# Kernel optimization log

Hardware: AMD Instinct MI355X
Metric: run time of the kernel (lower is better)

Reference implementation:

```python
import jax, jax.numpy as jnp
import numpy as np
from jax import lax

EPS = 1e-10

def _ln(x, g, b):
    m = x.mean(-1, keepdims=True)
    v = x.var(-1, keepdims=True)
    return (x - m) / jnp.sqrt(v + 1e-5) * g + b

def _gather(t, idx):
    # t: (B, HW, c), idx: (B, HW, d) -> (B, HW, d, c); out[n,i,k,:] = t[n, idx[n,i,k], :]
    return jax.vmap(lambda tn, In: tn[In])(t, idx)

def setup_inputs() -> dict:
    key = jax.random.key(0)
    ks = jax.random.split(key, 20)
    b, v, c, d, h, w, hid, ksz = 2, 2, 128, 64, 64, 64, 256, 5
    hw = h * w
    Bf = b * v  # v_1 == 1 target view per reference view
    std = 0.02
    return {
        'features_mv': jax.random.normal(ks[0], (b, v, c, h, w), jnp.float32),
        'warp_indices': jax.random.randint(ks[1], (Bf, hw, d), 0, hw, jnp.int32),
        'depth_prob': jax.random.uniform(ks[2], (Bf, hw, d), jnp.float32),
        'ln1_g': jnp.ones((c,), jnp.float32), 'ln1_b': jnp.zeros((c,), jnp.float32),
        'wq': jax.random.normal(ks[3], (c, c), jnp.float32) * std, 'bq': jnp.zeros((c,), jnp.float32),
        'wk': jax.random.normal(ks[4], (c, c), jnp.float32) * std, 'bk': jnp.zeros((c,), jnp.float32),
        'wv': jax.random.normal(ks[5], (c, c), jnp.float32) * std, 'bv': jnp.zeros((c,), jnp.float32),
        'k_pe': jax.random.normal(ks[6], (1, 1, d), jnp.float32) * std,
        'v_pe': jax.random.normal(ks[7], (1, 1, d), jnp.float32) * std,
        'rpe': jax.random.normal(ks[8], (1, 1, d), jnp.float32) * std,
        'proj_w': jax.random.normal(ks[9], (c, c), jnp.float32) * std, 'proj_b': jnp.zeros((c,), jnp.float32),
        'ln2_g': jnp.ones((c,), jnp.float32), 'ln2_b': jnp.zeros((c,), jnp.float32),
        'fc1_w': jax.random.normal(ks[10], (c, hid), jnp.float32) * std, 'fc1_b': jnp.zeros((hid,), jnp.float32),
        'dw_w': jax.random.normal(ks[11], (hid, 1, ksz, ksz), jnp.float32) * std, 'dw_b': jnp.zeros((hid,), jnp.float32),
        'fc2_w': jax.random.normal(ks[12], (hid, c), jnp.float32) * std, 'fc2_b': jnp.zeros((c,), jnp.float32),
    }

def reference(features_mv, warp_indices, depth_prob, ln1_g, ln1_b, wq, bq, wk, bk, wv, bv,
              k_pe, v_pe, rpe, proj_w, proj_b, ln2_g, ln2_b, fc1_w, fc1_b, dw_w, dw_b, fc2_w, fc2_b):
    b, v, c, h, w = features_mv.shape
    hw = h * w
    hid = fc1_w.shape[1]
    scale = c ** (-0.5)  # num_heads = 1 -> head_dim = dim

    # (b v) (h w) c
    x = features_mv.reshape(b * v, c, hw).transpose(0, 2, 1)
    shortcut = x
    xn = _ln(x, ln1_g, ln1_b)
    q = xn @ wq + bq
    k = xn @ wk + bk
    vv = xn @ wv + bv

    # nn pairing: v=2, v_1=1 -> each reference view attends the other view
    Q = (q.reshape(b, v, hw, c) * scale).reshape(b * v, hw, c)
    K = k.reshape(b, v, hw, c)[:, ::-1].reshape(b * v, hw, c)
    V = vv.reshape(b, v, hw, c)[:, ::-1].reshape(b * v, hw, c)

    # SMM_QmK: cost[n,i,k] = sum_c Q[n,i,c] * K[n, idx[n,i,k], c]
    Kg = _gather(K, warp_indices)                       # (B, hw, d, c)
    cost = jnp.einsum('bic,bikc->bik', Q, Kg)
    Q_pe = Q.sum(-1, keepdims=True)                     # (B, hw, 1)
    cost = cost + Q_pe * k_pe + rpe                     # broadcast (1,1,d)

    # (Sim_UNet similarity refinement omitted: UNetModel source unavailable; identity here)
    attn = jax.nn.softmax(cost, axis=-1)
    attn = attn * depth_prob
    attn = (attn + EPS) / (attn.sum(-1, keepdims=True) + EPS)

    # SMM_AmV: out[n,i,c] = sum_k attn[n,i,k] * V[n, idx[n,i,k], c]
    Vg = _gather(V, warp_indices)                       # (B, hw, d, c)
    out = jnp.einsum('bik,bikc->bic', attn, Vg)
    out = out + (attn * v_pe).sum(-1, keepdims=True)

    # projection + residual (v_1 == 1 so B == b*v)
    x = shortcut + (out @ proj_w + proj_b)

    # ConvFFN residual branch
    xn2 = _ln(x, ln2_g, ln2_b)
    y = jax.nn.gelu(xn2 @ fc1_w + fc1_b, approximate=False)
    yi = y.transpose(0, 2, 1).reshape(b * v, hid, h, w)
    yc = lax.conv_general_dilated(yi, dw_w, (1, 1), 'SAME', feature_group_count=hid,
                                  dimension_numbers=('NCHW', 'OIHW', 'NCHW'))
    yc = jax.nn.gelu(yc + dw_b[None, :, None, None], approximate=False)
    y = y + yc.reshape(b * v, hid, hw).transpose(0, 2, 1)
    y = y @ fc2_w + fc2_b
    return x + y
```

## Files before the change

### kernel.cpp

```cpp
#include <hip/hip_runtime.h>
#include <math.h>

#define TOK   16384
#define HW    4096
#define C     128
#define D     64
#define HID   256

constexpr float LN_EPS = 1e-5f;
constexpr float EPS_R  = 1e-10f;
constexpr float QSCALE = 0.08838834764831845f;

typedef __attribute__((ext_vector_type(8))) short  bf16x8;
typedef __attribute__((ext_vector_type(4))) float  f32x4;
#define MFMA16(a, b, c) __builtin_amdgcn_mfma_f32_16x16x32_bf16((a), (b), (c), 0, 0, 0)

__device__ __forceinline__ float bflo(unsigned u) { return __uint_as_float(u << 16); }
__device__ __forceinline__ float bfhi(unsigned u) { return __uint_as_float(u & 0xffff0000u); }
__device__ __forceinline__ float bfu(unsigned short u) { return __uint_as_float((unsigned)u << 16); }
__device__ __forceinline__ unsigned short f2bf(float f) {
  unsigned u = __float_as_uint(f);
  unsigned r = (u + 0x7fffu + ((u >> 16) & 1u)) >> 16;
  return (unsigned short)r;
}
__device__ __forceinline__ float gelu_exact(float x) {
  return 0.5f * x * (1.0f + erff(x * 0.7071067811865476f));
}

__global__ __launch_bounds__(256) void k_prep(const float* __restrict__ wq,
    const float* __restrict__ wk, const float* __restrict__ wv,
    const float* __restrict__ pw, const float* __restrict__ f1w,
    const float* __restrict__ f2w, unsigned short* __restrict__ wt) {
  int id = blockIdx.x * 256 + threadIdx.x;
  if (id < 16384) {
    int n = id >> 7, k = id & 127;
    wt[id] = f2bf(wq[k * 128 + n]);
  } else if (id < 32768) {
    int e = id - 16384; int n = e >> 7, k = e & 127;
    wt[id] = f2bf(wk[k * 128 + n]);
  } else if (id < 49152) {
    int e = id - 32768; int n = e >> 7, k = e & 127;
    wt[id] = f2bf(wv[k * 128 + n]);
  } else if (id < 65536) {
    int e = id - 49152; int n = e >> 7, k = e & 127;
    wt[id] = f2bf(pw[k * 128 + n]);
  } else if (id < 98304) {
    int e = id - 65536; int n = e >> 7, k = e & 127;
    wt[id] = f2bf(f1w[k * 256 + n]);
  } else if (id < 131072) {
    int e = id - 98304; int n = e >> 8, k = e & 255;
    wt[id] = f2bf(f2w[k * 128 + n]);
  }
}

__global__ __launch_bounds__(256) void k_ln1(const float* __restrict__ feat,
    const float* __restrict__ g, const float* __restrict__ b,
    unsigned short* __restrict__ xnb, float* __restrict__ xtm) {
  __shared__ float tile[64][C + 1];
  int t0 = blockIdx.x * 64;
  int n = t0 / HW, i0 = t0 % HW;
  int tid = threadIdx.x;
  const float* fb = feat + (size_t)n * C * HW;
  for (int e = tid; e < 64 * C; e += 256) {
    int ch = e >> 6, ii = e & 63;
    tile[ii][ch] = fb[(size_t)ch * HW + i0 + ii];
  }
  __syncthreads();
  int wave = tid >> 6, lane = tid & 63;
  for (int tkn = wave; tkn < 64; tkn += 4) {
    float a0 = tile[tkn][lane];
    float a1 = tile[tkn][lane + 64];
    float s = a0 + a1;
    for (int off = 32; off; off >>= 1) s += __shfl_xor(s, off, 64);
    float mean = s * (1.0f / 128.0f);
    float d0 = a0 - mean, d1 = a1 - mean;
    float v = d0 * d0 + d1 * d1;
    for (int off = 32; off; off >>= 1) v += __shfl_xor(v, off, 64);
    float rstd = rsqrtf(v * (1.0f / 128.0f) + LN_EPS);
    size_t ro = (size_t)(t0 + tkn) * C;
    xnb[ro + lane]      = f2bf(d0 * rstd * g[lane] + b[lane]);
    xnb[ro + lane + 64] = f2bf(d1 * rstd * g[lane + 64] + b[lane + 64]);
    xtm[ro + lane]      = a0;
    xtm[ro + lane + 64] = a1;
  }
}

__global__ __launch_bounds__(256) void k_qkv(const unsigned short* __restrict__ xnb,
    const unsigned short* __restrict__ wt,
    const float* __restrict__ bq, const float* __restrict__ bk,
    const float* __restrict__ bv, float* __restrict__ q,
    unsigned short* __restrict__ ksw, unsigned short* __restrict__ vsw) {
  int w = threadIdx.x >> 6, lane = threadIdx.x & 63;
  int q4 = lane >> 4, m = lane & 15;
  int t0 = blockIdx.x * 64 + w * 16;
  int wsel = blockIdx.y;
  const unsigned short* Wt = wt + wsel * 16384;
  const unsigned short* ap = xnb + (size_t)(t0 + m) * C + q4 * 8;
  bf16x8 a[4];
  #pragma unroll
  for (int ks = 0; ks < 4; ks++) a[ks] = *(const bf16x8*)(ap + ks * 32);
  f32x4 acc[8];
  #pragma unroll
  for (int nt = 0; nt < 8; nt++) acc[nt] = (f32x4){0.f, 0.f, 0.f, 0.f};
  #pragma unroll
  for (int nt = 0; nt < 8; nt++) {
    const unsigned short* bp = Wt + (size_t)(nt * 16 + m) * C + q4 * 8;
    #pragma unroll
    for (int ks = 0; ks < 4; ks++) {
      bf16x8 bfrag = *(const bf16x8*)(bp + ks * 32);
      acc[nt] = MFMA16(a[ks], bfrag, acc[nt]);
    }
  }
  if (wsel == 0) {
    #pragma unroll
    for (int nt = 0; nt < 8; nt++) {
      int col = nt * 16 + m;
      float bb = bq[col];
      #pragma unroll
      for (int reg = 0; reg < 4; reg++) {
        int row = t0 + q4 * 4 + reg;
        q[(size_t)row * C + col] = (acc[nt][reg] + bb) * QSCALE;
      }
    }
  } else {
    const float* B = (wsel == 1) ? bk : bv;
    unsigned short* O = (wsel == 1) ? ksw : vsw;
    int n = t0 >> 12, i0 = t0 & 4095;
    int tsw = ((n ^ 1) << 12) + i0;
    #pragma unroll
    for (int nt = 0; nt < 8; nt++) {
      int col = nt * 16 + m;
      float bb = B[col];
      #pragma unroll
      for (int reg = 0; reg < 4; reg++) {
        int row = tsw + q4 * 4 + reg;
        O[(size_t)row * C + col] = f2bf(acc[nt][reg] + bb);
      }
    }
  }
}

__global__ __launch_bounds__(256) void k_attn(const float* __restrict__ q,
    const unsigned short* __restrict__ ksw, const unsigned short* __restrict__ vsw,
    const int* __restrict__ widx, const float* __restrict__ dprob,
    const float* __restrict__ kpe, const float* __restrict__ vpe,
    const float* __restrict__ rpe, unsigned short* __restrict__ aoutb) {
  int lane = threadIdx.x & 63;
  int wave = threadIdx.x >> 6;
  int token = blockIdx.x * 4 + wave;
  int n = token >> 12;
  const unsigned short* Kb = ksw + (size_t)n * HW * C;
  const unsigned short* Vb = vsw + (size_t)n * HW * C;
  int g = lane >> 3, s = lane & 7;
  float qreg[16];
  const float* qp = q + (size_t)token * C + s * 16;
  #pragma unroll
  for (int i = 0; i < 4; i++) {
    float4 t = *(const float4*)(qp + i * 4);
    qreg[i * 4 + 0] = t.x; qreg[i * 4 + 1] = t.y;
    qreg[i * 4 + 2] = t.z; qreg[i * 4 + 3] = t.w;
  }
  float qpe = 0.f;
  #pragma unroll
  for (int i = 0; i < 16; i++) qpe += qreg[i];
  qpe += __shfl_xor(qpe, 1, 64);
  qpe += __shfl_xor(qpe, 2, 64);
  qpe += __shfl_xor(qpe, 4, 64);
  int myidx = widx[token * D + lane];
  float mydp = dprob[token * D + lane];
  float mycost = 0.f;
  #pragma unroll
  for (int pass = 0; pass < 8; ++pass) {
    int row = __shfl(myidx, pass * 8 + g, 64);
    const unsigned short* kr = Kb + (size_t)row * C + s * 16;
    uint4 ka = *(const uint4*)(kr);
    uint4 kb = *(const uint4*)(kr + 8);
    float p;
    p  = bflo(ka.x) * qreg[0]  + bfhi(ka.x) * qreg[1];
    p += bflo(ka.y) * qreg[2]  + bfhi(ka.y) * qreg[3];
    p += bflo(ka.z) * qreg[4]  + bfhi(ka.z) * qreg[5];
    p += bflo(ka.w) * qreg[6]  + bfhi(ka.w) * qreg[7];
    p += bflo(kb.x) * qreg[8]  + bfhi(kb.x) * qreg[9];
    p += bflo(kb.y) * qreg[10] + bfhi(kb.y) * qreg[11];
    p += bflo(kb.z) * qreg[12] + bfhi(kb.z) * qreg[13];
    p += bflo(kb.w) * qreg[14] + bfhi(kb.w) * qreg[15];
    p += __shfl_xor(p, 1, 64);
    p += __shfl_xor(p, 2, 64);
    p += __shfl_xor(p, 4, 64);
    float t = __shfl(p, (lane & 7) << 3, 64);
    if (pass == g) mycost = t;
  }
  mycost += qpe * kpe[lane] + rpe[lane];
  float mx = mycost;
  for (int off = 32; off; off >>= 1) mx = fmaxf(mx, __shfl_xor(mx, off, 64));
  float e = __expf(mycost - mx);
  float ssum = e;
  for (int off = 32; off; off >>= 1) ssum += __shfl_xor(ssum, off, 64);
  float attn = (e / ssum) * mydp;
  float s2 = attn;
  for (int off = 32; off; off >>= 1) s2 += __shfl_xor(s2, off, 64);
  attn = (attn + EPS_R) / (s2 + EPS_R);
  float vpt = attn * vpe[lane];
  for (int off = 32; off; off >>= 1) vpt += __shfl_xor(vpt, off, 64);
  float o0 = vpt, o1 = vpt;
  #pragma unroll 8
  for (int kk = 0; kk < D; ++kk) {
    int row = __shfl(myidx, kk, 64);
    float a = __shfl(attn, kk, 64);
    unsigned v = *(const unsigned*)(Vb + (size_t)row * C + lane * 2);
    o0 += a * bflo(v);
    o1 += a * bfhi(v);
  }
  unsigned pk = (unsigned)f2bf(o0) | ((unsigned)f2bf(o1) << 16);
  *(unsigned*)(aoutb + (size_t)token * C + lane * 2) = pk;
}

__global__ __launch_bounds__(256) void k_projln(const unsigned short* __restrict__ aoutb,
    const unsigned short* __restrict__ wt, const float* __restrict__ pb,
    float* __restrict__ xio, const float* __restrict__ g2,
    const float* __restrict__ b2, unsigned short* __restrict__ xn2b) {
  int w = threadIdx.x >> 6, lane = threadIdx.x & 63;
  int q4 = lane >> 4, m = lane & 15;
  int t0 = blockIdx.x * 64 + w * 16;
  const unsigned short* Wt = wt + 3 * 16384;
  const unsigned short* ap = aoutb + (size_t)(t0 + m) * C + q4 * 8;
  bf16x8 a[4];
  #pragma unroll
  for (int ks = 0; ks < 4; ks++) a[ks] = *(const bf16x8*)(ap + ks * 32);
  f32x4 acc[8];
  #pragma unroll
  for (int nt = 0; nt < 8; nt++) acc[nt] = (f32x4){0.f, 0.f, 0.f, 0.f};
  #pragma unroll
  for (int nt = 0; nt < 8; nt++) {
    const unsigned short* bp = Wt + (size_t)(nt * 16 + m) * C + q4 * 8;
    #pragma unroll
    for (int ks = 0; ks < 4; ks++) {
      bf16x8 bfrag = *(const bf16x8*)(bp + ks * 32);
      acc[nt] = MFMA16(a[ks], bfrag, acc[nt]);
    }
  }
  float s1[4] = {0.f, 0.f, 0.f, 0.f}, s2[4] = {0.f, 0.f, 0.f, 0.f};
  #pragma unroll
  for (int nt = 0; nt < 8; nt++) {
    int col = nt * 16 + m;
    float bb = pb[col];
    #pragma unroll
    for (int reg = 0; reg < 4; reg++) {
      int row = t0 + q4 * 4 + reg;
      float v = acc[nt][reg] + bb + xio[(size_t)row * C + col];
      acc[nt][reg] = v;
      s1[reg] += v;
      s2[reg] += v * v;
    }
  }
  #pragma unroll
  for (int reg = 0; reg < 4; reg++) {
    #pragma unroll
    for (int off = 1; off < 16; off <<= 1) {
      s1[reg] += __shfl_xor(s1[reg], off, 64);
      s2[reg] += __shfl_xor(s2[reg], off, 64);
    }
  }
  float mean[4], rstd[4];
  #pragma unroll
  for (int reg = 0; reg < 4; reg++) {
    mean[reg] = s1[reg] * (1.0f / 128.0f);
    float var = s2[reg] * (1.0f / 128.0f) - mean[reg] * mean[reg];
    rstd[reg] = rsqrtf(var + LN_EPS);
  }
  #pragma unroll
  for (int nt = 0; nt < 8; nt++) {
    int col = nt * 16 + m;
    float gc = g2[col], bc = b2[col];
    #pragma unroll
    for (int reg = 0; reg < 4; reg++) {
      int row = t0 + q4 * 4 + reg;
      float v = acc[nt][reg];
      xio[(size_t)row * C + col] = v;
      xn2b[(size_t)row * C + col] = f2bf((v - mean[reg]) * rstd[reg] * gc + bc);
    }
  }
}

__global__ __launch_bounds__(256) void k_fc1(const unsigned short* __restrict__ xn2b,
    const unsigned short* __restrict__ wt, const float* __restrict__ f1b,
    unsigned short* __restrict__ y) {
  int w = threadIdx.x >> 6, lane = threadIdx.x & 63;
  int q4 = lane >> 4, m = lane & 15;
  int t0 = blockIdx.x * 64 + w * 16;
  int n0 = blockIdx.y * 128;
  const unsigned short* Wt = wt + 65536 + (size_t)n0 * C;
  const unsigned short* ap = xn2b + (size_t)(t0 + m) * C + q4 * 8;
  bf16x8 a[4];
  #pragma unroll
  for (int ks = 0; ks < 4; ks++) a[ks] = *(const bf16x8*)(ap + ks * 32);
  f32x4 acc[8];
  #pragma unroll
  for (int nt = 0; nt < 8; nt++) acc[nt] = (f32x4){0.f, 0.f, 0.f, 0.f};
  #pragma unroll
  for (int nt = 0; nt < 8; nt++) {
    const unsigned short* bp = Wt + (size_t)(nt * 16 + m) * C + q4 * 8;
    #pragma unroll
    for (int ks = 0; ks < 4; ks++) {
      bf16x8 bfrag = *(const bf16x8*)(bp + ks * 32);
      acc[nt] = MFMA16(a[ks], bfrag, acc[nt]);
    }
  }
  #pragma unroll
  for (int nt = 0; nt < 8; nt++) {
    int col = n0 + nt * 16 + m;
    float bb = f1b[col];
    #pragma unroll
    for (int reg = 0; reg < 4; reg++) {
      int row = t0 + q4 * 4 + reg;
      y[(size_t)row * HID + col] = f2bf(gelu_exact(acc[nt][reg] + bb));
    }
  }
}

__global__ __launch_bounds__(256) void k_dwconv(const unsigned short* __restrict__ y,
    const float* __restrict__ w, const float* __restrict__ bias,
    unsigned short* __restrict__ yc) {
  __shared__ float tile[20 * 20][8];
  __shared__ float wl[8][25];
  __shared__ float bl[8];
  int bid = blockIdx.x;
  int tile_id = bid & 15;
  int cb = (bid >> 4) & 31;
  int n = bid >> 9;
  int ty = (tile_id >> 2) * 16, tx = (tile_id & 3) * 16;
  int ch0 = cb * 8;
  int tid = threadIdx.x;
  if (tid < 200) wl[tid / 25][tid % 25] = w[(size_t)(ch0 + tid / 25) * 25 + tid % 25];
  if (tid < 8) bl[tid] = bias[ch0 + tid];
  const unsigned short* yb = y + (size_t)n * HW * HID;
  for (int e = tid; e < 400 * 8; e += 256) {
    int cc = e & 7;
    int p = e >> 3;
    int py = p / 20, px = p % 20;
    int gy = ty + py - 2, gx = tx + px - 2;
    float v = 0.f;
    if (gy >= 0 && gy < 64 && gx >= 0 && gx < 64)
      v = bfu(yb[(size_t)(gy * 64 + gx) * HID + ch0 + cc]);
    tile[p][cc] = v;
  }
  __syncthreads();
  int cc = tid & 7;
  int xx = (tid >> 3) & 15;
  int yg = tid >> 7;
  float wreg[25];
  #pragma unroll
  for (int k = 0; k < 25; k++) wreg[k] = wl[cc][k];
  float bb = bl[cc];
  for (int j = 0; j < 8; ++j) {
    int yy = yg * 8 + j;
    float acc = 0.f;
    #pragma unroll
    for (int dy = 0; dy < 5; ++dy)
      #pragma unroll
      for (int dx = 0; dx < 5; ++dx)
        acc += wreg[dy * 5 + dx] * tile[(yy + dy) * 20 + (xx + dx)][cc];
    acc = gelu_exact(acc + bb);
    yc[(size_t)(n * HW + (ty + yy) * 64 + tx + xx) * HID + ch0 + cc] = f2bf(acc);
  }
}

__global__ __launch_bounds__(256) void k_fc2(const unsigned short* __restrict__ y,
    const unsigned short* __restrict__ ycg, const unsigned short* __restrict__ wt,
    const float* __restrict__ f2b, const float* __restrict__ xio,
    float* __restrict__ outp) {
  int w = threadIdx.x >> 6, lane = threadIdx.x & 63;
  int q4 = lane >> 4, m = lane & 15;
  int t0 = blockIdx.x * 64 + w * 16;
  const unsigned short* Wt = wt + 98304;
  const unsigned short* ap = y + (size_t)(t0 + m) * HID + q4 * 8;
  const unsigned short* cp = ycg + (size_t)(t0 + m) * HID + q4 * 8;
  union U { bf16x8 v; unsigned short s[8]; };
  bf16x8 a[8];
  #pragma unroll
  for (int ks = 0; ks < 8; ks++) {
    U ua, uc, ur;
    ua.v = *(const bf16x8*)(ap + ks * 32);
    uc.v = *(const bf16x8*)(cp + ks * 32);
    #pragma unroll
    for (int j = 0; j < 8; j++) ur.s[j] = f2bf(bfu(ua.s[j]) + bfu(uc.s[j]));
    a[ks] = ur.v;
  }
  f32x4 acc[8];
  #pragma unroll
  for (int nt = 0; nt < 8; nt++) acc[nt] = (f32x4){0.f, 0.f, 0.f, 0.f};
  #pragma unroll
  for (int nt = 0; nt < 8; nt++) {
    const unsigned short* bp = Wt + (size_t)(nt * 16 + m) * HID + q4 * 8;
    #pragma unroll
    for (int ks = 0; ks < 8; ks++) {
      bf16x8 bfrag = *(const bf16x8*)(bp + ks * 32);
      acc[nt] = MFMA16(a[ks], bfrag, acc[nt]);
    }
  }
  #pragma unroll
  for (int nt = 0; nt < 8; nt++) {
    int col = nt * 16 + m;
    float bb = f2b[col];
    #pragma unroll
    for (int reg = 0; reg < 4; reg++) {
      int row = t0 + q4 * 4 + reg;
      outp[(size_t)row * C + col] = acc[nt][reg] + bb + xio[(size_t)row * C + col];
    }
  }
}

extern "C" void kernel_launch(void* const* d_in, const int* in_sizes, int n_in,
                              void* d_out, int out_size, void* d_ws, size_t ws_size,
                              hipStream_t stream) {
  (void)in_sizes; (void)n_in; (void)out_size; (void)ws_size;
  const float* feat  = (const float*)d_in[0];
  const int*   widx  = (const int*)d_in[1];
  const float* dprob = (const float*)d_in[2];
  const float* ln1g  = (const float*)d_in[3];
  const float* ln1b  = (const float*)d_in[4];
  const float* wq    = (const float*)d_in[5];
  const float* bq    = (const float*)d_in[6];
  const float* wk    = (const float*)d_in[7];
  const float* bk    = (const float*)d_in[8];
  const float* wv    = (const float*)d_in[9];
  const float* bv    = (const float*)d_in[10];
  const float* kpe   = (const float*)d_in[11];
  const float* vpe   = (const float*)d_in[12];
  const float* rpe   = (const float*)d_in[13];
  const float* pw    = (const float*)d_in[14];
  const float* pb    = (const float*)d_in[15];
  const float* ln2g  = (const float*)d_in[16];
  const float* ln2b  = (const float*)d_in[17];
  const float* f1w   = (const float*)d_in[18];
  const float* f1b   = (const float*)d_in[19];
  const float* dww   = (const float*)d_in[20];
  const float* dwb   = (const float*)d_in[21];
  const float* f2w   = (const float*)d_in[22];
  const float* f2b   = (const float*)d_in[23];

  float* ws = (float*)d_ws;
  const size_t M2 = (size_t)TOK * C;
  float* qb  = ws;
  float* xio = ws + M2;
  unsigned short* xnb   = (unsigned short*)(ws + 2 * M2);
  unsigned short* ksb   = (unsigned short*)(ws + 2 * M2 + M2 / 2);
  unsigned short* vsb   = (unsigned short*)(ws + 3 * M2);
  unsigned short* aoutb = (unsigned short*)(ws + 3 * M2 + M2 / 2);
  unsigned short* xn2b  = (unsigned short*)(ws + 4 * M2);
  unsigned short* yb    = (unsigned short*)(ws + 4 * M2 + M2 / 2);
  unsigned short* ycgb  = (unsigned short*)(ws + 5 * M2 + M2 / 2);
  unsigned short* wtb   = (unsigned short*)(ws + 6 * M2 + M2 / 2);

  k_prep  <<<512, 256, 0, stream>>>(wq, wk, wv, pw, f1w, f2w, wtb);
  k_ln1   <<<TOK / 64, 256, 0, stream>>>(feat, ln1g, ln1b, xnb, xio);
  k_qkv   <<<dim3(TOK / 64, 3), 256, 0, stream>>>(xnb, wtb, bq, bk, bv, qb, ksb, vsb);
  k_attn  <<<TOK / 4, 256, 0, stream>>>(qb, ksb, vsb, widx, dprob, kpe, vpe, rpe, aoutb);
  k_projln<<<TOK / 64, 256, 0, stream>>>(aoutb, wtb, pb, xio, ln2g, ln2b, xn2b);
  k_fc1   <<<dim3(TOK / 64, 2), 256, 0, stream>>>(xn2b, wtb, f1b, yb);
  k_dwconv<<<2048, 256, 0, stream>>>(yb, dww, dwb, ycgb);
  k_fc2   <<<TOK / 64, 256, 0, stream>>>(yb, ycgb, wtb, f2b, xio, (float*)d_out);
}
```

Before: 222.2 us.

## Fuse LN1 into QKV and LN2 into FC1, reorder attention blocks, use readlane

LayerNorm1 is merged with the QKV GEMM, so the normalized activations stay in shared memory instead of going through a global bf16 buffer. Likewise proj+LN2 is merged with FC1, which now computes all 256 hidden columns per block. The attention kernel remaps block indices to interleave the four batch images across blocks, and its gather loop now uses readlane broadcasts with full unrolling. This cuts two kernel launches and two intermediate tensor round trips. The cost is fewer blocks per fused GEMM, higher register pressure (16 accumulators in FC1) and serial QKV work within each block.

```diff
diff --git a/kernel.cpp b/kernel.cpp
--- a/kernel.cpp
+++ b/kernel.cpp
@@ -53,12 +53,17 @@
   }
 }
 
-__global__ __launch_bounds__(256) void k_ln1(const float* __restrict__ feat,
+__global__ __launch_bounds__(256) void k_ln1qkv(const float* __restrict__ feat,
     const float* __restrict__ g, const float* __restrict__ b,
-    unsigned short* __restrict__ xnb, float* __restrict__ xtm) {
+    const unsigned short* __restrict__ wt,
+    const float* __restrict__ bq, const float* __restrict__ bk,
+    const float* __restrict__ bv, float* __restrict__ q,
+    unsigned short* __restrict__ ksw, unsigned short* __restrict__ vsw,
+    float* __restrict__ xtm) {
   __shared__ float tile[64][C + 1];
-  int t0 = blockIdx.x * 64;
-  int n = t0 / HW, i0 = t0 % HW;
+  __shared__ unsigned short xs[64][136];
+  int tb = blockIdx.x * 64;
+  int n = tb / HW, i0 = tb % HW;
   int tid = threadIdx.x;
   const float* fb = feat + (size_t)n * C * HW;
   for (int e = tid; e < 64 * C; e += 256) {
@@ -66,8 +71,8 @@
     tile[ii][ch] = fb[(size_t)ch * HW + i0 + ii];
   }
   __syncthreads();
-  int wave = tid >> 6, lane = tid & 63;
-  for (int tkn = wave; tkn < 64; tkn += 4) {
+  int w = tid >> 6, lane = tid & 63;
+  for (int tkn = w; tkn < 64; tkn += 4) {
     float a0 = tile[tkn][lane];
     float a1 = tile[tkn][lane + 64];
     float s = a0 + a1;
@@ -77,64 +82,58 @@
     float v = d0 * d0 + d1 * d1;
     for (int off = 32; off; off >>= 1) v += __shfl_xor(v, off, 64);
     float rstd = rsqrtf(v * (1.0f / 128.0f) + LN_EPS);
-    size_t ro = (size_t)(t0 + tkn) * C;
-    xnb[ro + lane]      = f2bf(d0 * rstd * g[lane] + b[lane]);
-    xnb[ro + lane + 64] = f2bf(d1 * rstd * g[lane + 64] + b[lane + 64]);
+    size_t ro = (size_t)(tb + tkn) * C;
+    xs[tkn][lane]      = f2bf(d0 * rstd * g[lane] + b[lane]);
+    xs[tkn][lane + 64] = f2bf(d1 * rstd * g[lane + 64] + b[lane + 64]);
     xtm[ro + lane]      = a0;
     xtm[ro + lane + 64] = a1;
   }
-}
-
-__global__ __launch_bounds__(256) void k_qkv(const unsigned short* __restrict__ xnb,
-    const unsigned short* __restrict__ wt,
-    const float* __restrict__ bq, const float* __restrict__ bk,
-    const float* __restrict__ bv, float* __restrict__ q,
-    unsigned short* __restrict__ ksw, unsigned short* __restrict__ vsw) {
-  int w = threadIdx.x >> 6, lane = threadIdx.x & 63;
+  __syncthreads();
   int q4 = lane >> 4, m = lane & 15;
-  int t0 = blockIdx.x * 64 + w * 16;
-  int wsel = blockIdx.y;
-  const unsigned short* Wt = wt + wsel * 16384;
-  const unsigned short* ap = xnb + (size_t)(t0 + m) * C + q4 * 8;
+  int t0 = tb + w * 16;
   bf16x8 a[4];
   #pragma unroll
-  for (int ks = 0; ks < 4; ks++) a[ks] = *(const bf16x8*)(ap + ks * 32);
-  f32x4 acc[8];
-  #pragma unroll
-  for (int nt = 0; nt < 8; nt++) acc[nt] = (f32x4){0.f, 0.f, 0.f, 0.f};
-  #pragma unroll
-  for (int nt = 0; nt < 8; nt++) {
-    const unsigned short* bp = Wt + (size_t)(nt * 16 + m) * C + q4 * 8;
-    #pragma unroll
-    for (int ks = 0; ks < 4; ks++) {
-      bf16x8 bfrag = *(const bf16x8*)(bp + ks * 32);
-      acc[nt] = MFMA16(a[ks], bfrag, acc[nt]);
-    }
-  }
-  if (wsel == 0) {
+  for (int ks = 0; ks < 4; ks++)
+    a[ks] = *(const bf16x8*)(&xs[w * 16 + m][ks * 32 + q4 * 8]);
+  int tsw = ((n ^ 1) << 12) + i0 + w * 16;
+  #pragma unroll
+  for (int wsel = 0; wsel < 3; ++wsel) {
+    const unsigned short* Wt = wt + wsel * 16384;
+    f32x4 acc[8];
+    #pragma unroll
+    for (int nt = 0; nt < 8; nt++) acc[nt] = (f32x4){0.f, 0.f, 0.f, 0.f};
     #pragma unroll
     for (int nt = 0; nt < 8; nt++) {
-      int col = nt * 16 + m;
-      float bb = bq[col];
+      const unsigned short* bp = Wt + (size_t)(nt * 16 + m) * C + q4 * 8;
       #pragma unroll
-      for (int reg = 0; reg < 4; reg++) {
-        int row = t0 + q4 * 4 + reg;
-        q[(size_t)row * C + col] = (acc[nt][reg] + bb) * QSCALE;
+      for (int ks = 0; ks < 4; ks++) {
+        bf16x8 bfrag = *(const bf16x8*)(bp + ks * 32);
+        acc[nt] = MFMA16(a[ks], bfrag, acc[nt]);
       }
     }
-  } else {
-    const float* B = (wsel == 1) ? bk : bv;
-    unsigned short* O = (wsel == 1) ? ksw : vsw;
-    int n = t0 >> 12, i0 = t0 & 4095;
-    int tsw = ((n ^ 1) << 12) + i0;
-    #pragma unroll
-    for (int nt = 0; nt < 8; nt++) {
-      int col = nt * 16 + m;
-      float bb = B[col];
+    if (wsel == 0) {
       #pragma unroll
-      for (int reg = 0; reg < 4; reg++) {
-        int row = tsw + q4 * 4 + reg;
-        O[(size_t)row * C + col] = f2bf(acc[nt][reg] + bb);
+      for (int nt = 0; nt < 8; nt++) {
+        int col = nt * 16 + m;
+        float bb = bq[col];
+        #pragma unroll
+        for (int reg = 0; reg < 4; reg++) {
+          int row = t0 + q4 * 4 + reg;
+          q[(size_t)row * C + col] = (acc[nt][reg] + bb) * QSCALE;
+        }
+      }
+    } else {
+      const float* B = (wsel == 1) ? bk : bv;
+      unsigned short* O = (wsel == 1) ? ksw : vsw;
+      #pragma unroll
+      for (int nt = 0; nt < 8; nt++) {
+        int col = nt * 16 + m;
+        float bb = B[col];
+        #pragma unroll
+        for (int reg = 0; reg < 4; reg++) {
+          int row = tsw + q4 * 4 + reg;
+          O[(size_t)row * C + col] = f2bf(acc[nt][reg] + bb);
+        }
       }
     }
   }
@@ -147,8 +146,10 @@
     const float* __restrict__ rpe, unsigned short* __restrict__ aoutb) {
   int lane = threadIdx.x & 63;
   int wave = threadIdx.x >> 6;
-  int token = blockIdx.x * 4 + wave;
-  int n = token >> 12;
+  int bid = blockIdx.x;
+  int n = (bid >> 1) & 3;
+  int within = ((bid >> 3) << 1) | (bid & 1);
+  int token = n * HW + within * 4 + wave;
   const unsigned short* Kb = ksw + (size_t)n * HW * C;
   const unsigned short* Vb = vsw + (size_t)n * HW * C;
   int g = lane >> 3, s = lane & 7;
@@ -203,10 +204,11 @@
   float vpt = attn * vpe[lane];
   for (int off = 32; off; off >>= 1) vpt += __shfl_xor(vpt, off, 64);
   float o0 = vpt, o1 = vpt;
-  #pragma unroll 8
+  unsigned att_u = __float_as_uint(attn);
+  #pragma unroll
   for (int kk = 0; kk < D; ++kk) {
-    int row = __shfl(myidx, kk, 64);
-    float a = __shfl(attn, kk, 64);
+    int row = __builtin_amdgcn_readlane(myidx, kk);
+    float a = __uint_as_float(__builtin_amdgcn_readlane(att_u, kk));
     unsigned v = *(const unsigned*)(Vb + (size_t)row * C + lane * 2);
     o0 += a * bflo(v);
     o1 += a * bfhi(v);
@@ -215,13 +217,16 @@
   *(unsigned*)(aoutb + (size_t)token * C + lane * 2) = pk;
 }
 
-__global__ __launch_bounds__(256) void k_projln(const unsigned short* __restrict__ aoutb,
+__global__ __launch_bounds__(256) void k_projfc1(const unsigned short* __restrict__ aoutb,
     const unsigned short* __restrict__ wt, const float* __restrict__ pb,
     float* __restrict__ xio, const float* __restrict__ g2,
-    const float* __restrict__ b2, unsigned short* __restrict__ xn2b) {
+    const float* __restrict__ b2, const float* __restrict__ f1b,
+    unsigned short* __restrict__ y) {
+  __shared__ unsigned short xs[64][136];
   int w = threadIdx.x >> 6, lane = threadIdx.x & 63;
   int q4 = lane >> 4, m = lane & 15;
-  int t0 = blockIdx.x * 64 + w * 16;
+  int tb = blockIdx.x * 64;
+  int t0 = tb + w * 16;
   const unsigned short* Wt = wt + 3 * 16384;
   const unsigned short* ap = aoutb + (size_t)(t0 + m) * C + q4 * 8;
   bf16x8 a[4];
@@ -261,13 +266,6 @@
       s2[reg] += __shfl_xor(s2[reg], off, 64);
     }
   }
-  float mean[4], rstd[4];
-  #pragma unroll
-  for (int reg = 0; reg < 4; reg++) {
-    mean[reg] = s1[reg] * (1.0f / 128.0f);
-    float var = s2[reg] * (1.0f / 128.0f) - mean[reg] * mean[reg];
-    rstd[reg] = rsqrtf(var + LN_EPS);
-  }
   #pragma unroll
   for (int nt = 0; nt < 8; nt++) {
     int col = nt * 16 + m;
@@ -275,45 +273,40 @@
     #pragma unroll
     for (int reg = 0; reg < 4; reg++) {
       int row = t0 + q4 * 4 + reg;
+      float mean = s1[reg] * (1.0f / 128.0f);
+      float var = s2[reg] * (1.0f / 128.0f) - mean * mean;
+      float rstd = rsqrtf(var + LN_EPS);
       float v = acc[nt][reg];
       xio[(size_t)row * C + col] = v;
-      xn2b[(size_t)row * C + col] = f2bf((v - mean[reg]) * rstd[reg] * gc + bc);
-    }
-  }
-}
-
-__global__ __launch_bounds__(256) void k_fc1(const unsigned short* __restrict__ xn2b,
-    const unsigned short* __restrict__ wt, const float* __restrict__ f1b,
-    unsigned short* __restrict__ y) {
-  int w = threadIdx.x >> 6, lane = threadIdx.x & 63;
-  int q4 = lane >> 4, m = lane & 15;
-  int t0 = blockIdx.x * 64 + w * 16;
-  int n0 = blockIdx.y * 128;
-  const unsigned short* Wt = wt + 65536 + (size_t)n0 * C;
-  const unsigned short* ap = xn2b + (size_t)(t0 + m) * C + q4 * 8;
-  bf16x8 a[4];
-  #pragma unroll
-  for (int ks = 0; ks < 4; ks++) a[ks] = *(const bf16x8*)(ap + ks * 32);
-  f32x4 acc[8];
-  #pragma unroll
-  for (int nt = 0; nt < 8; nt++) acc[nt] = (f32x4){0.f, 0.f, 0.f, 0.f};
-  #pragma unroll
-  for (int nt = 0; nt < 8; nt++) {
-    const unsigned short* bp = Wt + (size_t)(nt * 16 + m) * C + q4 * 8;
+      xs[w * 16 + q4 * 4 + reg][col] = f2bf((v - mean) * rstd * gc + bc);
+    }
+  }
+  __syncthreads();
+  const unsigned short* Wf = wt + 65536;
+  bf16x8 a2[4];
+  #pragma unroll
+  for (int ks = 0; ks < 4; ks++)
+    a2[ks] = *(const bf16x8*)(&xs[w * 16 + m][ks * 32 + q4 * 8]);
+  f32x4 acc2[16];
+  #pragma unroll
+  for (int nt = 0; nt < 16; nt++) acc2[nt] = (f32x4){0.f, 0.f, 0.f, 0.f};
+  #pragma unroll
+  for (int nt = 0; nt < 16; nt++) {
+    const unsigned short* bp = Wf + (size_t)(nt * 16 + m) * C + q4 * 8;
     #pragma unroll
     for (int ks = 0; ks < 4; ks++) {
       bf16x8 bfrag = *(const bf16x8*)(bp + ks * 32);
-      acc[nt] = MFMA16(a[ks], bfrag, acc[nt]);
-    }
-  }
-  #pragma unroll
-  for (int nt = 0; nt < 8; nt++) {
-    int col = n0 + nt * 16 + m;
+      acc2[nt] = MFMA16(a2[ks], bfrag, acc2[nt]);
+    }
+  }
+  #pragma unroll
+  for (int nt = 0; nt < 16; nt++) {
+    int col = nt * 16 + m;
     float bb = f1b[col];
     #pragma unroll
     for (int reg = 0; reg < 4; reg++) {
       int row = t0 + q4 * 4 + reg;
-      y[(size_t)row * HID + col] = f2bf(gelu_exact(acc[nt][reg] + bb));
+      y[(size_t)row * HID + col] = f2bf(gelu_exact(acc2[nt][reg] + bb));
     }
   }
 }
@@ -443,21 +436,17 @@
   const size_t M2 = (size_t)TOK * C;
   float* qb  = ws;
   float* xio = ws + M2;
-  unsigned short* xnb   = (unsigned short*)(ws + 2 * M2);
-  unsigned short* ksb   = (unsigned short*)(ws + 2 * M2 + M2 / 2);
-  unsigned short* vsb   = (unsigned short*)(ws + 3 * M2);
-  unsigned short* aoutb = (unsigned short*)(ws + 3 * M2 + M2 / 2);
-  unsigned short* xn2b  = (unsigned short*)(ws + 4 * M2);
-  unsigned short* yb    = (unsigned short*)(ws + 4 * M2 + M2 / 2);
-  unsigned short* ycgb  = (unsigned short*)(ws + 5 * M2 + M2 / 2);
-  unsigned short* wtb   = (unsigned short*)(ws + 6 * M2 + M2 / 2);
-
-  k_prep  <<<512, 256, 0, stream>>>(wq, wk, wv, pw, f1w, f2w, wtb);
-  k_ln1   <<<TOK / 64, 256, 0, stream>>>(feat, ln1g, ln1b, xnb, xio);
-  k_qkv   <<<dim3(TOK / 64, 3), 256, 0, stream>>>(xnb, wtb, bq, bk, bv, qb, ksb, vsb);
-  k_attn  <<<TOK / 4, 256, 0, stream>>>(qb, ksb, vsb, widx, dprob, kpe, vpe, rpe, aoutb);
-  k_projln<<<TOK / 64, 256, 0, stream>>>(aoutb, wtb, pb, xio, ln2g, ln2b, xn2b);
-  k_fc1   <<<dim3(TOK / 64, 2), 256, 0, stream>>>(xn2b, wtb, f1b, yb);
-  k_dwconv<<<2048, 256, 0, stream>>>(yb, dww, dwb, ycgb);
-  k_fc2   <<<TOK / 64, 256, 0, stream>>>(yb, ycgb, wtb, f2b, xio, (float*)d_out);
-}
+  unsigned short* ksb   = (unsigned short*)(ws + 2 * M2);
+  unsigned short* vsb   = (unsigned short*)(ws + 2 * M2 + M2 / 2);
+  unsigned short* aoutb = (unsigned short*)(ws + 3 * M2);
+  unsigned short* yb    = (unsigned short*)(ws + 3 * M2 + M2 / 2);
+  unsigned short* ycgb  = (unsigned short*)(ws + 4 * M2 + M2 / 2);
+  unsigned short* wtb   = (unsigned short*)(ws + 5 * M2 + M2 / 2);
+
+  k_prep   <<<512, 256, 0, stream>>>(wq, wk, wv, pw, f1w, f2w, wtb);
+  k_ln1qkv <<<TOK / 64, 256, 0, stream>>>(feat, ln1g, ln1b, wtb, bq, bk, bv, qb, ksb, vsb, xio);
+  k_attn   <<<TOK / 4, 256, 0, stream>>>(qb, ksb, vsb, widx, dprob, kpe, vpe, rpe, aoutb);
+  k_projfc1<<<TOK / 64, 256, 0, stream>>>(aoutb, wtb, pb, xio, ln2g, ln2b, f1b, yb);
+  k_dwconv <<<2048, 256, 0, stream>>>(yb, dww, dwb, ycgb);
+  k_fc2    <<<TOK / 64, 256, 0, stream>>>(yb, ycgb, wtb, f2b, xio, (float*)d_out);
+}
```

Measured after the change: 227.0 us. 1.02x slower.

## Batch K/V gather loads, interleave attention blocks across batches, pad dwconv tile

Applied to the files above, without the earlier changes.

In the attention kernel, all eight K-row gathers are issued before any dot products, and the V gather is split into blocks of eight loads issued ahead of the FMAs. Row indices and attention weights are broadcast with readlane instead of shuffles. Block indices are remapped so that neighbouring blocks cover different batch images, which spreads the gather traffic. The dwconv shared tile is transposed to channel-major with padding to change the LDS bank access pattern. The aim is more memory-level parallelism for the random gathers, at the cost of higher register pressure.

```diff
diff --git a/kernel.cpp b/kernel.cpp
--- a/kernel.cpp
+++ b/kernel.cpp
@@ -147,11 +147,15 @@
     const float* __restrict__ rpe, unsigned short* __restrict__ aoutb) {
   int lane = threadIdx.x & 63;
   int wave = threadIdx.x >> 6;
-  int token = blockIdx.x * 4 + wave;
-  int n = token >> 12;
+  int bid = blockIdx.x;
+  int n = (bid >> 1) & 3;
+  int within = ((bid >> 3) << 1) | (bid & 1);
+  int token = n * HW + within * 4 + wave;
   const unsigned short* Kb = ksw + (size_t)n * HW * C;
   const unsigned short* Vb = vsw + (size_t)n * HW * C;
   int g = lane >> 3, s = lane & 7;
+  int myidx = widx[token * D + lane];
+  float mydp = dprob[token * D + lane];
   float qreg[16];
   const float* qp = q + (size_t)token * C + s * 16;
   #pragma unroll
@@ -166,24 +170,29 @@
   qpe += __shfl_xor(qpe, 1, 64);
   qpe += __shfl_xor(qpe, 2, 64);
   qpe += __shfl_xor(qpe, 4, 64);
-  int myidx = widx[token * D + lane];
-  float mydp = dprob[token * D + lane];
+  int rowv[8];
+  #pragma unroll
+  for (int pass = 0; pass < 8; ++pass)
+    rowv[pass] = __shfl(myidx, pass * 8 + g, 64);
+  uint4 ka[8], kb[8];
+  #pragma unroll
+  for (int pass = 0; pass < 8; ++pass) {
+    const unsigned short* kr = Kb + (size_t)rowv[pass] * C + s * 16;
+    ka[pass] = *(const uint4*)(kr);
+    kb[pass] = *(const uint4*)(kr + 8);
+  }
   float mycost = 0.f;
   #pragma unroll
   for (int pass = 0; pass < 8; ++pass) {
-    int row = __shfl(myidx, pass * 8 + g, 64);
-    const unsigned short* kr = Kb + (size_t)row * C + s * 16;
-    uint4 ka = *(const uint4*)(kr);
-    uint4 kb = *(const uint4*)(kr + 8);
     float p;
-    p  = bflo(ka.x) * qreg[0]  + bfhi(ka.x) * qreg[1];
-    p += bflo(ka.y) * qreg[2]  + bfhi(ka.y) * qreg[3];
-    p += bflo(ka.z) * qreg[4]  + bfhi(ka.z) * qreg[5];
-    p += bflo(ka.w) * qreg[6]  + bfhi(ka.w) * qreg[7];
-    p += bflo(kb.x) * qreg[8]  + bfhi(kb.x) * qreg[9];
-    p += bflo(kb.y) * qreg[10] + bfhi(kb.y) * qreg[11];
-    p += bflo(kb.z) * qreg[12] + bfhi(kb.z) * qreg[13];
-    p += bflo(kb.w) * qreg[14] + bfhi(kb.w) * qreg[15];
+    p  = bflo(ka[pass].x) * qreg[0]  + bfhi(ka[pass].x) * qreg[1];
+    p += bflo(ka[pass].y) * qreg[2]  + bfhi(ka[pass].y) * qreg[3];
+    p += bflo(ka[pass].z) * qreg[4]  + bfhi(ka[pass].z) * qreg[5];
+    p += bflo(ka[pass].w) * qreg[6]  + bfhi(ka[pass].w) * qreg[7];
+    p += bflo(kb[pass].x) * qreg[8]  + bfhi(kb[pass].x) * qreg[9];
+    p += bflo(kb[pass].y) * qreg[10] + bfhi(kb[pass].y) * qreg[11];
+    p += bflo(kb[pass].z) * qreg[12] + bfhi(kb[pass].z) * qreg[13];
+    p += bflo(kb[pass].w) * qreg[14] + bfhi(kb[pass].w) * qreg[15];
     p += __shfl_xor(p, 1, 64);
     p += __shfl_xor(p, 2, 64);
     p += __shfl_xor(p, 4, 64);
@@ -203,13 +212,21 @@
   float vpt = attn * vpe[lane];
   for (int off = 32; off; off >>= 1) vpt += __shfl_xor(vpt, off, 64);
   float o0 = vpt, o1 = vpt;
-  #pragma unroll 8
-  for (int kk = 0; kk < D; ++kk) {
-    int row = __shfl(myidx, kk, 64);
-    float a = __shfl(attn, kk, 64);
-    unsigned v = *(const unsigned*)(Vb + (size_t)row * C + lane * 2);
-    o0 += a * bflo(v);
-    o1 += a * bfhi(v);
+  unsigned att_u = __float_as_uint(attn);
+  #pragma unroll
+  for (int blk = 0; blk < 8; ++blk) {
+    unsigned vv[8];
+    #pragma unroll
+    for (int j = 0; j < 8; j++) {
+      int row = __builtin_amdgcn_readlane(myidx, blk * 8 + j);
+      vv[j] = *(const unsigned*)(Vb + (size_t)row * C + lane * 2);
+    }
+    #pragma unroll
+    for (int j = 0; j < 8; j++) {
+      float a = __uint_as_float(__builtin_amdgcn_readlane(att_u, blk * 8 + j));
+      o0 += a * bflo(vv[j]);
+      o1 += a * bfhi(vv[j]);
+    }
   }
   unsigned pk = (unsigned)f2bf(o0) | ((unsigned)f2bf(o1) << 16);
   *(unsigned*)(aoutb + (size_t)token * C + lane * 2) = pk;
@@ -321,7 +338,7 @@
 __global__ __launch_bounds__(256) void k_dwconv(const unsigned short* __restrict__ y,
     const float* __restrict__ w, const float* __restrict__ bias,
     unsigned short* __restrict__ yc) {
-  __shared__ float tile[20 * 20][8];
+  __shared__ float tile[8][401];
   __shared__ float wl[8][25];
   __shared__ float bl[8];
   int bid = blockIdx.x;
@@ -342,7 +359,7 @@
     float v = 0.f;
     if (gy >= 0 && gy < 64 && gx >= 0 && gx < 64)
       v = bfu(yb[(size_t)(gy * 64 + gx) * HID + ch0 + cc]);
-    tile[p][cc] = v;
+    tile[cc][p] = v;
   }
   __syncthreads();
   int cc = tid & 7;
@@ -359,7 +376,7 @@
     for (int dy = 0; dy < 5; ++dy)
       #pragma unroll
       for (int dx = 0; dx < 5; ++dx)
-        acc += wreg[dy * 5 + dx] * tile[(yy + dy) * 20 + (xx + dx)][cc];
+        acc += wreg[dy * 5 + dx] * tile[cc][(yy + dy) * 20 + (xx + dx)];
     acc = gelu_exact(acc + bb);
     yc[(size_t)(n * HW + (ty + yy) * 64 + tx + xx) * HID + ch0 + cc] = f2bf(acc);
   }
```

Result: faster. 217.3 us (-2.2%).
